# Kernel tuning notes

Hardware: AMD Instinct MI355X
Metric: run time of the kernel (lower is better)

The kernel has to match this reference:

```python
import jax, jax.numpy as jnp
import numpy as np
import math

C = 1.0          # Poincare ball curvature
MIN_NORM = 1e-15
BALL_EPS = 1e-5  # clamp for artanh args


def _norm(x):
    return jnp.sqrt(jnp.maximum(jnp.sum(x * x, -1, keepdims=True), MIN_NORM))


def expmap0(u, c=C):
    sc = jnp.sqrt(c)
    n = _norm(u)
    return jnp.tanh(sc * n) * u / (sc * n)


def logmap0(x, c=C):
    sc = jnp.sqrt(c)
    n = _norm(x)
    return jnp.arctanh(jnp.minimum(sc * n, 1.0 - BALL_EPS)) * x / (sc * n)


def mobius_add(x, y, c=C):
    x2 = jnp.sum(x * x, -1, keepdims=True)
    y2 = jnp.sum(y * y, -1, keepdims=True)
    xy = jnp.sum(x * y, -1, keepdims=True)
    num = (1.0 + 2.0 * c * xy + c * y2) * x + (1.0 - c * x2) * y
    den = 1.0 + 2.0 * c * xy + c * c * x2 * y2
    return num / jnp.maximum(den, MIN_NORM)


def mobius_matvec(W, x, c=C):
    # W: (out, in), x: (..., in)
    sc = jnp.sqrt(c)
    xn = _norm(x)
    mx = x @ W.T
    mxn = _norm(mx)
    return jnp.tanh(mxn / xn * jnp.arctanh(jnp.minimum(sc * xn, 1.0 - BALL_EPS))) * mx / (mxn * sc)


def mobius_scalar_mul(r, x, c=C):
    sc = jnp.sqrt(c)
    n = _norm(x)
    return jnp.tanh(r * jnp.arctanh(jnp.minimum(sc * n, 1.0 - BALL_EPS))) * x / (n * sc)


def hyp_linear(x, W, b):
    return mobius_add(mobius_matvec(W, x), b)


def layer_norm(t, w, b, eps=1e-5):
    mu = jnp.mean(t, -1, keepdims=True)
    var = jnp.mean((t - mu) ** 2, -1, keepdims=True)
    return (t - mu) / jnp.sqrt(var + eps) * w + b


def hyp_layer_norm(x, w, b):
    return expmap0(layer_norm(logmap0(x), w, b))


def _hyperbolic_attention_scores(q, k, c=C, epsilon=1e-15, delta=1e-7):
    # q, k: (B, H, S, Dh)
    max_norm = (1.0 - 1e-5) / math.sqrt(c)
    q = jnp.minimum(q, max_norm)  # elementwise clamp_max, faithful to torch
    k = jnp.minimum(k, max_norm)
    q_norm_sq = c * jnp.sum(q * q, -1, keepdims=True)          # (B,H,Sq,1)
    k_norm_sq = c * jnp.sum(k * k, -1, keepdims=True)          # (B,H,Sk,1)
    # diff: (B,H,Sq,Sk,Dh) = mobius_add(-k, q) pairwise
    diff = mobius_add(-k[:, :, None, :, :], q[:, :, :, None, :], c)
    diff_norm_sq = c * jnp.sum(diff * diff, -1)                # (B,H,Sq,Sk)
    denom = (1.0 - q_norm_sq) * (1.0 - jnp.swapaxes(k_norm_sq, 2, 3)) + epsilon
    acosh_arg = 1.0 + 2.0 * diff_norm_sq / denom
    acosh_arg = jnp.maximum(acosh_arg, 1.0 + delta)
    dist = jnp.log(acosh_arg + jnp.sqrt(acosh_arg * acosh_arg - 1.0))
    return -dist


def setup_inputs() -> dict:
    key = jax.random.key(0)
    D, H, FF = 768, 12, 4 * 768
    B, S = 2, 196
    ks = jax.random.split(key, 8)

    def xavier(k, out_f, in_f):
        lim = math.sqrt(6.0 / (in_f + out_f))
        return jax.random.uniform(k, (out_f, in_f), jnp.float32, -lim, lim)

    x = jax.random.normal(ks[0], (B, S, D), jnp.float32) * 0.02  # inside unit ball
    return {
        "x": x,
        "wq": xavier(ks[1], D, D), "bq": jnp.zeros((D,), jnp.float32),
        "wk": xavier(ks[2], D, D), "bk": jnp.zeros((D,), jnp.float32),
        "wv": xavier(ks[3], D, D), "bv": jnp.zeros((D,), jnp.float32),
        "wo": xavier(ks[4], D, D), "bo": jnp.zeros((D,), jnp.float32),
        "head_scaling": jnp.ones((H, 1, 1), jnp.float32),
        "w1": xavier(ks[5], FF, D), "b1": jnp.zeros((FF,), jnp.float32),
        "w2": xavier(ks[6], D, FF), "b2": jnp.zeros((D,), jnp.float32),
        "beta": jnp.ones((1,), jnp.float32),
        "ln1_w": jnp.ones((D,), jnp.float32), "ln1_b": jnp.zeros((D,), jnp.float32),
        "ln2_w": jnp.ones((D,), jnp.float32), "ln2_b": jnp.zeros((D,), jnp.float32),
    }


def reference(x, wq, bq, wk, bk, wv, bv, wo, bo, head_scaling,
              w1, b1, w2, b2, beta, ln1_w, ln1_b, ln2_w, ln2_b):
    B, S, D = x.shape
    H = head_scaling.shape[0]
    Dh = D // H

    # --- hyperbolic multi-head attention ---
    q = hyp_linear(x, wq, bq)
    k = hyp_linear(x, wk, bk)
    v = hyp_linear(x, wv, bv)
    q = jnp.transpose(q.reshape(B, S, H, Dh), (0, 2, 1, 3))
    k = jnp.transpose(k.reshape(B, S, H, Dh), (0, 2, 1, 3))
    v = jnp.transpose(v.reshape(B, S, H, Dh), (0, 2, 1, 3))

    scores = _hyperbolic_attention_scores(q, k) / (head_scaling * math.sqrt(Dh))
    attn = jax.nn.softmax(scores, axis=-1)                       # (B,H,Sq,Sk)
    attn_out = expmap0(jnp.einsum('bhqk,bhkd->bhqd', attn, logmap0(v)))
    attn_out = jnp.transpose(attn_out, (0, 2, 1, 3)).reshape(B, S, D)
    attn_out = hyp_linear(attn_out, wo, bo)

    # --- residual 1 + hyperbolic layer norm ---
    h = mobius_add(x, mobius_scalar_mul(beta, attn_out))
    h = hyp_layer_norm(h, ln1_w, ln1_b)

    # --- mobius FFN ---
    f = hyp_linear(h, w1, b1)
    f = expmap0(jax.nn.relu(logmap0(f)))   # mobius_relu
    f = hyp_linear(f, w2, b2)

    # --- residual 2 + hyperbolic layer norm ---
    out = mobius_add(h, mobius_scalar_mul(beta, f))
    out = hyp_layer_norm(out, ln2_w, ln2_b)
    return out
```

## Files before the change

kernel.cpp:

```cpp
#include <hip/hip_runtime.h>
#include <hip/hip_bf16.h>
#include <math.h>

#define BATCH 2
#define SEQ 196
#define DMODEL 768
#define NHEAD 12
#define DHEAD 64
#define DFF 3072
#define NROWS (BATCH*SEQ)
#define NBH   (BATCH*NHEAD)
#define NHROWS (NBH*SEQ)

typedef __attribute__((ext_vector_type(8))) short short8;
typedef __attribute__((ext_vector_type(4))) float f32x4;

__device__ __forceinline__ short f2bf(float f) {
  unsigned u = __builtin_bit_cast(unsigned, f);
  u += 0x7FFFu + ((u >> 16) & 1u);
  return (short)(u >> 16);
}
__device__ __forceinline__ float bf2f(short s) {
  unsigned u = ((unsigned)(unsigned short)s) << 16;
  return __builtin_bit_cast(float, u);
}
__device__ __forceinline__ float wave_sum64(float v) {
  #pragma unroll
  for (int off = 32; off; off >>= 1) v += __shfl_xor(v, off);
  return v;
}

__device__ __forceinline__ void block_reduce_sum4(float& a, float& b, float& c, float& d,
                                                  float* sbuf ) {
  #pragma unroll
  for (int off = 32; off; off >>= 1) {
    a += __shfl_xor(a, off);
    b += __shfl_xor(b, off);
    c += __shfl_xor(c, off);
    d += __shfl_xor(d, off);
  }
  int wid = threadIdx.x >> 6;
  if ((threadIdx.x & 63) == 0) {
    sbuf[wid*4+0] = a; sbuf[wid*4+1] = b; sbuf[wid*4+2] = c; sbuf[wid*4+3] = d;
  }
  __syncthreads();
  a = sbuf[0] + sbuf[4] + sbuf[8]  + sbuf[12];
  b = sbuf[1] + sbuf[5] + sbuf[9]  + sbuf[13];
  c = sbuf[2] + sbuf[6] + sbuf[10] + sbuf[14];
  d = sbuf[3] + sbuf[7] + sbuf[11] + sbuf[15];
  __syncthreads();
}

#define PITCH 72

__global__ __launch_bounds__(256) void gemm_qkv_f32(
    const float* __restrict__ X,
    const float* __restrict__ Wq, const float* __restrict__ Wk, const float* __restrict__ Wv,
    float* __restrict__ Yq, float* __restrict__ Yk, float* __restrict__ Yv) {
  const float* W = Wq; float* Y = Yq;
  if (blockIdx.z == 1) { W = Wk; Y = Yk; }
  else if (blockIdx.z == 2) { W = Wv; Y = Yv; }
  const int K = DMODEL, m = DMODEL, n = NROWS;

  __shared__ short As[64*PITCH];
  __shared__ short Bs[64*PITCH];
  const int tid  = threadIdx.x;
  const int lane = tid & 63;
  const int w    = tid >> 6, wr = w >> 1, wc = w & 1;
  const int brow = blockIdx.y * 64, bcol = blockIdx.x * 64;

  const int sr = tid >> 2, sc = (tid & 3) * 16;
  const bool rok = (brow + sr) < n;
  const float* xp = X + (size_t)(brow + sr) * K + sc;
  const float* wp = W + (size_t)(bcol + sr) * K + sc;

  f32x4 acc[2][2] = {};
  const int kgo = (lane >> 4) * 8;
  const f32x4 zf = {0.f,0.f,0.f,0.f};

  f32x4 xa[4], wa[4];
  #pragma unroll
  for (int q = 0; q < 4; ++q) {
    xa[q] = rok ? *(const f32x4*)(xp + q*4) : zf;
    wa[q] = *(const f32x4*)(wp + q*4);
  }

  const int T = K / 64;
  for (int t = 0; t < T; ++t) {
    f32x4 xn[4], wn[4];
    const int kn = (t + 1 < T) ? (t + 1) * 64 : 0;
    #pragma unroll
    for (int q = 0; q < 4; ++q) {
      xn[q] = rok ? *(const f32x4*)(xp + kn + q*4) : zf;
      wn[q] = *(const f32x4*)(wp + kn + q*4);
    }

    short8 xs0, xs1, ws0, ws1;
    #pragma unroll
    for (int j = 0; j < 4; ++j) {
      xs0[j] = f2bf(xa[0][j]); xs0[j+4] = f2bf(xa[1][j]);
      xs1[j] = f2bf(xa[2][j]); xs1[j+4] = f2bf(xa[3][j]);
      ws0[j] = f2bf(wa[0][j]); ws0[j+4] = f2bf(wa[1][j]);
      ws1[j] = f2bf(wa[2][j]); ws1[j+4] = f2bf(wa[3][j]);
    }
    __syncthreads();
    *(short8*)&As[sr*PITCH + sc]     = xs0;
    *(short8*)&As[sr*PITCH + sc + 8] = xs1;
    *(short8*)&Bs[sr*PITCH + sc]     = ws0;
    *(short8*)&Bs[sr*PITCH + sc + 8] = ws1;
    __syncthreads();

    #pragma unroll
    for (int kk = 0; kk < 2; ++kk) {
      short8 a0 = *(const short8*)&As[(wr*32      + (lane & 15))*PITCH + kk*32 + kgo];
      short8 a1 = *(const short8*)&As[(wr*32 + 16 + (lane & 15))*PITCH + kk*32 + kgo];
      short8 b0 = *(const short8*)&Bs[(wc*32      + (lane & 15))*PITCH + kk*32 + kgo];
      short8 b1 = *(const short8*)&Bs[(wc*32 + 16 + (lane & 15))*PITCH + kk*32 + kgo];
      acc[0][0] = __builtin_amdgcn_mfma_f32_16x16x32_bf16(a0, b0, acc[0][0], 0, 0, 0);
      acc[0][1] = __builtin_amdgcn_mfma_f32_16x16x32_bf16(a0, b1, acc[0][1], 0, 0, 0);
      acc[1][0] = __builtin_amdgcn_mfma_f32_16x16x32_bf16(a1, b0, acc[1][0], 0, 0, 0);
      acc[1][1] = __builtin_amdgcn_mfma_f32_16x16x32_bf16(a1, b1, acc[1][1], 0, 0, 0);
    }
    #pragma unroll
    for (int q = 0; q < 4; ++q) { xa[q] = xn[q]; wa[q] = wn[q]; }
  }

  const int ccol = bcol + wc*32 + (lane & 15);
  #pragma unroll
  for (int mr = 0; mr < 2; ++mr) {
    #pragma unroll
    for (int j = 0; j < 4; ++j) {
      int grow = brow + wr*32 + mr*16 + (lane >> 4)*4 + j;
      if (grow < n) {
        float* yr = Y + (size_t)grow * m + ccol;
        yr[0]  = acc[mr][0][j];
        yr[16] = acc[mr][1][j];
      }
    }
  }
}

__global__ __launch_bounds__(256) void gemm_awf32(
    const short* __restrict__ A, const float* __restrict__ W,
    float* __restrict__ Yparts, int n, int Ktot, int m, int KK) {
  const int z = blockIdx.z;
  const int kbase = z * KK;
  float* Y = Yparts + (size_t)z * n * m;

  __shared__ short As[64*PITCH];
  __shared__ short Bs[64*PITCH];
  const int tid  = threadIdx.x;
  const int lane = tid & 63;
  const int w    = tid >> 6, wr = w >> 1, wc = w & 1;
  const int brow = blockIdx.y * 64, bcol = blockIdx.x * 64;

  const int sr = tid >> 2, sc = (tid & 3) * 16;
  const bool rok = (brow + sr) < n;
  const short* ap = A + (size_t)(brow + sr) * Ktot + kbase + sc;
  const float* wp = W + (size_t)(bcol + sr) * Ktot + kbase + sc;

  f32x4 acc[2][2] = {};
  const int kgo = (lane >> 4) * 8;
  const short8 z8 = {0,0,0,0,0,0,0,0};
  const f32x4 zf = {0.f,0.f,0.f,0.f};

  short8 aa0, aa1;
  f32x4 wa[4];
  if (rok) { aa0 = *(const short8*)(ap); aa1 = *(const short8*)(ap + 8); }
  else     { aa0 = z8; aa1 = z8; }
  #pragma unroll
  for (int q = 0; q < 4; ++q) wa[q] = *(const f32x4*)(wp + q*4);

  const int T = KK / 64;
  for (int t = 0; t < T; ++t) {
    short8 an0, an1;
    f32x4 wn[4];
    const int kn = (t + 1 < T) ? (t + 1) * 64 : 0;
    if (rok) { an0 = *(const short8*)(ap + kn); an1 = *(const short8*)(ap + kn + 8); }
    else     { an0 = z8; an1 = z8; }
    #pragma unroll
    for (int q = 0; q < 4; ++q) wn[q] = *(const f32x4*)(wp + kn + q*4);

    short8 ws0, ws1;
    #pragma unroll
    for (int j = 0; j < 4; ++j) {
      ws0[j] = f2bf(wa[0][j]); ws0[j+4] = f2bf(wa[1][j]);
      ws1[j] = f2bf(wa[2][j]); ws1[j+4] = f2bf(wa[3][j]);
    }
    __syncthreads();
    *(short8*)&As[sr*PITCH + sc]     = aa0;
    *(short8*)&As[sr*PITCH + sc + 8] = aa1;
    *(short8*)&Bs[sr*PITCH + sc]     = ws0;
    *(short8*)&Bs[sr*PITCH + sc + 8] = ws1;
    __syncthreads();

    #pragma unroll
    for (int kk = 0; kk < 2; ++kk) {
      short8 a0 = *(const short8*)&As[(wr*32      + (lane & 15))*PITCH + kk*32 + kgo];
      short8 a1 = *(const short8*)&As[(wr*32 + 16 + (lane & 15))*PITCH + kk*32 + kgo];
      short8 b0 = *(const short8*)&Bs[(wc*32      + (lane & 15))*PITCH + kk*32 + kgo];
      short8 b1 = *(const short8*)&Bs[(wc*32 + 16 + (lane & 15))*PITCH + kk*32 + kgo];
      acc[0][0] = __builtin_amdgcn_mfma_f32_16x16x32_bf16(a0, b0, acc[0][0], 0, 0, 0);
      acc[0][1] = __builtin_amdgcn_mfma_f32_16x16x32_bf16(a0, b1, acc[0][1], 0, 0, 0);
      acc[1][0] = __builtin_amdgcn_mfma_f32_16x16x32_bf16(a1, b0, acc[1][0], 0, 0, 0);
      acc[1][1] = __builtin_amdgcn_mfma_f32_16x16x32_bf16(a1, b1, acc[1][1], 0, 0, 0);
    }
    aa0 = an0; aa1 = an1;
    #pragma unroll
    for (int q = 0; q < 4; ++q) wa[q] = wn[q];
  }

  const int ccol = bcol + wc*32 + (lane & 15);
  #pragma unroll
  for (int mr = 0; mr < 2; ++mr) {
    #pragma unroll
    for (int j = 0; j < 4; ++j) {
      int grow = brow + wr*32 + mr*16 + (lane >> 4)*4 + j;
      if (grow < n) {
        float* yr = Y + (size_t)grow * m + ccol;
        yr[0]  = acc[mr][0][j];
        yr[16] = acc[mr][1][j];
      }
    }
  }
}

#define P_P 256
__global__ __launch_bounds__(256) void qkv_post(const float* __restrict__ X,
                                                const float* __restrict__ MQ,
                                                const float* __restrict__ MK,
                                                const float* __restrict__ MV,
                                                const float* __restrict__ bq,
                                                const float* __restrict__ bk,
                                                const float* __restrict__ bv,
                                                short* __restrict__ qhb,
                                                short* __restrict__ khb,
                                                float* __restrict__ q2s,
                                                float* __restrict__ k2s,
                                                short* __restrict__ lvT) {
  __shared__ float sbuf[16];
  const int r = blockIdx.x;
  const int b = r / SEQ, s = r % SEQ;
  const int y = blockIdx.y;
  const float* MX   = (y == 0) ? MQ : (y == 1) ? MK : MV;
  const float* bias = (y == 0) ? bq : (y == 1) ? bk : bv;
  const float* xr = X + (size_t)r*DMODEL;
  const float* mr = MX + (size_t)r*DMODEL;
  const int tid = threadIdx.x, wid = tid >> 6, lane = tid & 63;
  const float maxn = 1.0f - 1e-5f;

  float xs = 0.f, ms = 0.f, mb = 0.f, bb = 0.f;
  float mv[3], bvv[3];
  #pragma unroll
  for (int l = 0; l < 3; ++l) {
    int i = tid + l*256;
    float xv = xr[i];
    mv[l] = mr[i]; bvv[l] = bias[i];
    xs += xv*xv; ms += mv[l]*mv[l]; mb += mv[l]*bvv[l]; bb += bvv[l]*bvv[l];
  }
  block_reduce_sum4(xs, ms, mb, bb, sbuf);
  float xn  = sqrtf(fmaxf(xs, 1e-15f));
  float mxn = sqrtf(fmaxf(ms, 1e-15f));
  float art = atanhf(fminf(xn, maxn));
  float scm = tanhf(mxn/xn*art)/mxn;
  float x2 = scm*scm*ms;
  float y2 = bb;
  float xy = scm*mb;
  float den = fmaxf(1.f + 2.f*xy + x2*y2, 1e-15f);
  float ca = (1.f + 2.f*xy + y2) * scm / den;
  float cb = (1.f - x2) / den;

  #pragma unroll
  for (int l = 0; l < 3; ++l) {
    float o = ca*mv[l] + cb*bvv[l];
    int h = l*4 + wid;
    size_t hr = (size_t)(b*NHEAD + h)*SEQ + s;
    if (y < 2) {
      short c16 = f2bf(fminf(o, maxn));
      float cf = bf2f(c16);
      float nn = wave_sum64(cf*cf);
      if (y == 0) {
        qhb[hr*64 + lane] = c16;
        if (lane == 0) q2s[hr] = nn;
      } else {
        khb[hr*64 + lane] = c16;
        if (lane == 0) k2s[hr] = nn;
      }
    } else {
      float nn = wave_sum64(o*o);
      float n = sqrtf(fmaxf(nn, 1e-15f));
      float scl = atanhf(fminf(n, maxn))/n;
      lvT[((size_t)(b*NHEAD + h)*DHEAD + lane)*P_P + s] = f2bf(scl*o);
    }
  }
}

#define SP 72
#define PP 264
__global__ __launch_bounds__(256) void attn_mfma(
    const short* __restrict__ qhb, const short* __restrict__ khb,
    const float* __restrict__ q2s, const float* __restrict__ k2s,
    const short* __restrict__ lvT, const float* __restrict__ hs,
    short* __restrict__ aob) {
  __shared__ __align__(16) char smem[9216 + 224*SP*2];
  __shared__ float q2l[64];
  __shared__ float k2l[224];
  __shared__ float redA[64][2];
  __shared__ float redB[64][2];

  const int tile = blockIdx.x, bh = blockIdx.z;
  const int h = bh % NHEAD, b = bh / NHEAD;
  const int i0 = tile*64;
  const int tid = threadIdx.x, lane = tid & 63, w = tid >> 6, wr = w >> 1, wc = w & 1;
  short* Qs = (short*)smem;
  short* Ks = (short*)(smem + 9216);
  short* Pl = (short*)smem;
  const short8 z8 = {0,0,0,0,0,0,0,0};
  const int kgo = (lane >> 4)*8;

  {
    int row = tid >> 2, seg = (tid & 3)*16;
    int gr = i0 + row;
    short8 v0 = z8, v1 = z8;
    if (gr < SEQ) {
      const short* p = qhb + ((size_t)bh*SEQ + gr)*64 + seg;
      v0 = *(const short8*)p; v1 = *(const short8*)(p + 8);
    }
    *(short8*)&Qs[row*SP + seg]     = v0;
    *(short8*)&Qs[row*SP + seg + 8] = v1;
  }
  for (int u = tid; u < 224*4; u += 256) {
    int row = u >> 2, seg = (u & 3)*16;
    short8 v0 = z8, v1 = z8;
    if (row < SEQ) {
      const short* p = khb + ((size_t)bh*SEQ + row)*64 + seg;
      v0 = *(const short8*)p; v1 = *(const short8*)(p + 8);
    }
    *(short8*)&Ks[row*SP + seg]     = v0;
    *(short8*)&Ks[row*SP + seg + 8] = v1;
  }
  if (tid < 64)  q2l[tid] = (i0 + tid < SEQ) ? q2s[(size_t)bh*SEQ + i0 + tid] : 0.f;
  if (tid < 224) k2l[tid] = (tid < SEQ) ? k2s[(size_t)bh*SEQ + tid] : 0.f;
  __syncthreads();

  f32x4 acc[2][7] = {};
  #pragma unroll
  for (int kk = 0; kk < 2; ++kk) {
    short8 a0 = *(const short8*)&Qs[(wr*32      + (lane & 15))*SP + kk*32 + kgo];
    short8 a1 = *(const short8*)&Qs[(wr*32 + 16 + (lane & 15))*SP + kk*32 + kgo];
// ... 5 lines not shown
    }
  }

  const float inv_hsv = 1.f/(hs[h]*8.0f);
  #pragma unroll
  for (int rf = 0; rf < 2; ++rf) {
    #pragma unroll
    for (int j = 0; j < 4; ++j) {
      int rl = wr*32 + rf*16 + (lane >> 4)*4 + j;
      float q2 = q2l[rl];
      #pragma unroll
      for (int cf = 0; cf < 7; ++cf) {
        int col = wc*112 + cf*16 + (lane & 15);
        float kq = acc[rf][cf][j];
        float k2 = k2l[col];
        float xy = -kq;
        float al = 1.f + 2.f*xy + q2;
        float be = 1.f - k2;
        float num2 = al*al*k2 + 2.f*al*be*xy + be*be*q2;
        float den  = fmaxf(1.f + 2.f*xy + k2*q2, 1e-15f);
        float dns  = num2/(den*den);
        float denom = (1.f - q2)*(1.f - k2) + 1e-15f;
        float arg = fmaxf(1.f + 2.f*dns/denom, 1.f + 1e-7f);
        float dist = logf(arg + sqrtf(arg*arg - 1.f));
        acc[rf][cf][j] = (col < SEQ) ? -dist*inv_hsv : -1e30f;
      }
      float m = acc[rf][0][j];
      #pragma unroll
      for (int cf = 1; cf < 7; ++cf) m = fmaxf(m, acc[rf][cf][j]);
      m = fmaxf(m, __shfl_xor(m, 1));
      m = fmaxf(m, __shfl_xor(m, 2));
      m = fmaxf(m, __shfl_xor(m, 4));
      m = fmaxf(m, __shfl_xor(m, 8));
      if ((lane & 15) == 0) redA[rl][wc] = m;
    }
  }
  __syncthreads();

  #pragma unroll
  for (int rf = 0; rf < 2; ++rf) {
    #pragma unroll
    for (int j = 0; j < 4; ++j) {
      int rl = wr*32 + rf*16 + (lane >> 4)*4 + j;
      float m = fmaxf(redA[rl][0], redA[rl][1]);
      float s = 0.f;
      #pragma unroll
      for (int cf = 0; cf < 7; ++cf) {
        float e = expf(acc[rf][cf][j] - m);
        acc[rf][cf][j] = e;
        s += e;
      }
      s += __shfl_xor(s, 1); s += __shfl_xor(s, 2);
      s += __shfl_xor(s, 4); s += __shfl_xor(s, 8);
      if ((lane & 15) == 0) redB[rl][wc] = s;
    }
  }
  __syncthreads();

  #pragma unroll
  for (int rf = 0; rf < 2; ++rf) {
    #pragma unroll
    for (int j = 0; j < 4; ++j) {
      int rl = wr*32 + rf*16 + (lane >> 4)*4 + j;
      float inv = 1.f/(redB[rl][0] + redB[rl][1]);
      #pragma unroll
      for (int cf = 0; cf < 7; ++cf) {
        int col = wc*112 + cf*16 + (lane & 15);
        Pl[rl*PP + col] = f2bf(acc[rf][cf][j]*inv);
      }
    }
  }
  __syncthreads();

  f32x4 acc2[2][2] = {};
  const short* lvb = lvT + (size_t)bh*DHEAD*P_P;
  #pragma unroll
  for (int ks = 0; ks < 7; ++ks) {
    short8 a0 = *(const short8*)&Pl[(wr*32      + (lane & 15))*PP + ks*32 + kgo];
    short8 a1 = *(const short8*)&Pl[(wr*32 + 16 + (lane & 15))*PP + ks*32 + kgo];
    short8 b0 = *(const short8*)(lvb + (size_t)(wc*32      + (lane & 15))*P_P + ks*32 + kgo);
    short8 b1 = *(const short8*)(lvb + (size_t)(wc*32 + 16 + (lane & 15))*P_P + ks*32 + kgo);
    acc2[0][0] = __builtin_amdgcn_mfma_f32_16x16x32_bf16(a0, b0, acc2[0][0], 0, 0, 0);
    acc2[0][1] = __builtin_amdgcn_mfma_f32_16x16x32_bf16(a0, b1, acc2[0][1], 0, 0, 0);
    acc2[1][0] = __builtin_amdgcn_mfma_f32_16x16x32_bf16(a1, b0, acc2[1][0], 0, 0, 0);
    acc2[1][1] = __builtin_amdgcn_mfma_f32_16x16x32_bf16(a1, b1, acc2[1][1], 0, 0, 0);
  }

  #pragma unroll
  for (int rf = 0; rf < 2; ++rf) {
    #pragma unroll
    for (int j = 0; j < 4; ++j) {
      int rl = wr*32 + rf*16 + (lane >> 4)*4 + j;
      float s = acc2[rf][0][j]*acc2[rf][0][j] + acc2[rf][1][j]*acc2[rf][1][j];
      s += __shfl_xor(s, 1); s += __shfl_xor(s, 2);
      s += __shfl_xor(s, 4); s += __shfl_xor(s, 8);
      if ((lane & 15) == 0) redA[rl][wc] = s;
    }
  }
  __syncthreads();

  #pragma unroll
  for (int rf = 0; rf < 2; ++rf) {
    #pragma unroll
    for (int j = 0; j < 4; ++j) {
      int rl = wr*32 + rf*16 + (lane >> 4)*4 + j;
      int grow = i0 + rl;
      if (grow < SEQ) {
        float n2 = redA[rl][0] + redA[rl][1];
        float n = sqrtf(fmaxf(n2, 1e-15f));
        float scl = tanhf(n)/n;
        #pragma unroll
        for (int cf2 = 0; cf2 < 2; ++cf2) {
          int col = h*64 + wc*32 + cf2*16 + (lane & 15);
          float o = scl*acc2[rf][cf2][j];
          aob[(size_t)(b*SEQ + grow)*DMODEL + col] = f2bf(o);
        }
      }
    }
  }
}

__global__ __launch_bounds__(256) void post_resid_ln(
    const short* __restrict__ Xbf, const float* __restrict__ xsArr, int din,
    const float* __restrict__ MXp, int nparts,
    const float* __restrict__ bias, const float* __restrict__ RX,
    const float* __restrict__ betap, const float* __restrict__ lnw,
    const float* __restrict__ lnb,
    float* __restrict__ out, short* __restrict__ outb) {
  __shared__ float sbuf[16];
  const int r = blockIdx.x;
  const int tid = threadIdx.x;

  float xs = 0.f, ms = 0.f, mb = 0.f, bb = 0.f;
  float mv[3], bvv[3];
  #pragma unroll
  for (int l = 0; l < 3; ++l) {
    int i = tid + l*256;
    float acc = 0.f;
    for (int p = 0; p < nparts; ++p)
      acc += MXp[(size_t)p*NROWS*DMODEL + (size_t)r*DMODEL + i];
    mv[l] = acc; bvv[l] = bias[i];
    ms += mv[l]*mv[l]; mb += mv[l]*bvv[l]; bb += bvv[l]*bvv[l];
  }
  if (Xbf) {
    const short* xr = Xbf + (size_t)r*din;
    for (int i = tid; i < din; i += 256) { float v = bf2f(xr[i]); xs += v*v; }
  }
  block_reduce_sum4(xs, ms, mb, bb, sbuf);
  if (!Xbf) xs = xsArr[r];

  float xn  = sqrtf(fmaxf(xs, 1e-15f));
  float mxn = sqrtf(fmaxf(ms, 1e-15f));
  float art = atanhf(fminf(xn, 1.f - 1e-5f));
  float scm = tanhf(mxn/xn*art)/mxn;
  float px2 = scm*scm*ms;
  float py2 = bb;
  float pxy = scm*mb;
  float pden = fmaxf(1.f + 2.f*pxy + px2*py2, 1e-15f);
  float pca = (1.f + 2.f*pxy + py2) * scm / pden;
  float pcb = (1.f - px2) / pden;

  const float* xr2 = RX + (size_t)r*DMODEL;
  float xv[3], yv[3];
// ... 22 lines not shown
  float z1 = 0.f, z2 = 0.f, z3 = 0.f;
  block_reduce_sum4(h2, z1, z2, z3, sbuf);

  float nh = sqrtf(fmaxf(h2, 1e-15f));
  float scl = atanhf(fminf(nh, 1.f - 1e-5f))/nh;
  float tv[3]; float tsum = 0.f, tsq = 0.f;
  #pragma unroll
  for (int l = 0; l < 3; ++l) { tv[l] = scl*hv[l]; tsum += tv[l]; tsq += tv[l]*tv[l]; }
  float zz = 0.f, zw = 0.f;
  block_reduce_sum4(tsum, tsq, zz, zw, sbuf);
  float mu  = tsum * (1.f/768.f);
  float var = tsq * (1.f/768.f) - mu*mu;
  float rstd = rsqrtf(var + 1e-5f);
  float lnv[3]; float l2 = 0.f;
  #pragma unroll
  for (int l = 0; l < 3; ++l) {
    int i = tid + l*256;
    lnv[l] = (tv[l] - mu)*rstd*lnw[i] + lnb[i];
    l2 += lnv[l]*lnv[l];
  }
  float w1 = 0.f, w2 = 0.f, w3 = 0.f;
  block_reduce_sum4(l2, w1, w2, w3, sbuf);
  float nl = sqrtf(fmaxf(l2, 1e-15f));
  float sce = tanhf(nl)/nl;
  #pragma unroll
  for (int l = 0; l < 3; ++l) {
    int i = tid + l*256;
    float o = sce*lnv[l];
    out[(size_t)r*DMODEL + i] = o;
    if (outb) outb[(size_t)r*DMODEL + i] = f2bf(o);
  }
}

__global__ __launch_bounds__(256) void ffn1_post(const float* __restrict__ hb,
                                                 const float* __restrict__ MX,
                                                 const float* __restrict__ bias,
                                                 short* __restrict__ fbb,
                                                 float* __restrict__ fnorm) {
  __shared__ float sbuf[16];
  const int r = blockIdx.x;
  const int tid = threadIdx.x;
  const float* xr = hb + (size_t)r*DMODEL;
  const float* mr = MX + (size_t)r*DFF;

  float xs = 0.f, ms = 0.f, mb = 0.f, bb = 0.f;
  float mv[12], bvv[12];
  for (int i = tid; i < DMODEL; i += 256) { float v = xr[i]; xs += v*v; }
  #pragma unroll
  for (int l = 0; l < 12; ++l) {
    int i = tid + l*256;
    mv[l] = mr[i]; bvv[l] = bias[i];
    ms += mv[l]*mv[l]; mb += mv[l]*bvv[l]; bb += bvv[l]*bvv[l];
  }
  block_reduce_sum4(xs, ms, mb, bb, sbuf);
  float xn  = sqrtf(fmaxf(xs, 1e-15f));
  float mxn = sqrtf(fmaxf(ms, 1e-15f));
  float art = atanhf(fminf(xn, 1.f - 1e-5f));
  float scm = tanhf(mxn/xn*art)/mxn;
  float px2 = scm*scm*ms;
  float py2 = bb;
  float pxy = scm*mb;
  float pden = fmaxf(1.f + 2.f*pxy + px2*py2, 1e-15f);
  float pca = (1.f + 2.f*pxy + py2) * scm / pden;
  float pcb = (1.f - px2) / pden;

  float s2 = pca*pca*ms + 2.f*pca*pcb*mb + pcb*pcb*bb;
  float n = sqrtf(fmaxf(s2, 1e-15f));
  float scl = atanhf(fminf(n, 1.f - 1e-5f))/n;
  float rv[12]; float r2 = 0.f;
  #pragma unroll
  for (int l = 0; l < 12; ++l) {
    float f = pca*mv[l] + pcb*bvv[l];
    rv[l] = fmaxf(scl*f, 0.f);
    r2 += rv[l]*rv[l];
  }
  float w1 = 0.f, w2 = 0.f, w3 = 0.f;
  block_reduce_sum4(r2, w1, w2, w3, sbuf);
  float nr = sqrtf(fmaxf(r2, 1e-15f));
  float sce = tanhf(nr)/nr;
  #pragma unroll
  for (int l = 0; l < 12; ++l)
    fbb[(size_t)r*DFF + tid + l*256] = f2bf(sce*rv[l]);
  if (tid == 0) fnorm[r] = sce*sce*r2;
}

extern "C" void kernel_launch(void* const* d_in, const int* in_sizes, int n_in,
                              void* d_out, int out_size, void* d_ws, size_t ws_size,
                              hipStream_t stream) {
  const float* x    = (const float*)d_in[0];
  const float* wq   = (const float*)d_in[1];
  const float* bq   = (const float*)d_in[2];
  const float* wk   = (const float*)d_in[3];
  const float* bk   = (const float*)d_in[4];
  const float* wv   = (const float*)d_in[5];
  const float* bv   = (const float*)d_in[6];
  const float* wo   = (const float*)d_in[7];
  const float* bo   = (const float*)d_in[8];
  const float* hs   = (const float*)d_in[9];
  const float* w1   = (const float*)d_in[10];
  const float* b1   = (const float*)d_in[11];
  const float* w2   = (const float*)d_in[12];
  const float* b2   = (const float*)d_in[13];
  const float* beta = (const float*)d_in[14];
  const float* ln1w = (const float*)d_in[15];
  const float* ln1b = (const float*)d_in[16];
  const float* ln2w = (const float*)d_in[17];
  const float* ln2b = (const float*)d_in[18];
  float* out = (float*)d_out;

  char* base = (char*)d_ws;
  size_t off = 0;
  auto allocB = [&](size_t bytes) {
    off = (off + 63) & ~(size_t)63;
    void* p = base + off; off += bytes; return p;
  };
  short* aob  = (short*)allocB((size_t)NROWS*DMODEL * 2);
  short* hbb  = (short*)allocB((size_t)NROWS*DMODEL * 2);
  short* fbb  = (short*)allocB((size_t)NROWS*DFF * 2);
  float* tq   = (float*)allocB((size_t)NROWS*DMODEL * 4);
  float* tk   = (float*)allocB((size_t)NROWS*DMODEL * 4);
  float* tv   = (float*)allocB((size_t)NROWS*DMODEL * 4);
  float* gparts = (float*)allocB((size_t)4*NROWS*DMODEL * 4);
  short* qhb  = (short*)allocB((size_t)NHROWS*DHEAD * 2);
  short* khb  = (short*)allocB((size_t)NHROWS*DHEAD * 2);
  float* q2s  = (float*)allocB((size_t)NHROWS * 4);
  float* k2s  = (float*)allocB((size_t)NHROWS * 4);
  short* lvT  = (short*)allocB((size_t)NBH*DHEAD*P_P * 2);
  float* hb   = (float*)allocB((size_t)NROWS*DMODEL * 4);
  float* tmpF = (float*)allocB((size_t)NROWS*DFF * 4);
  float* fnorm= (float*)allocB((size_t)NROWS * 4);

  dim3 blk(256);
  dim3 gQKV(DMODEL/64, (NROWS+63)/64, 3);
  dim3 gO(DMODEL/64,   (NROWS+63)/64, 2);
  dim3 gF1(DFF/64,     (NROWS+63)/64, 1);
  dim3 gF2(DMODEL/64,  (NROWS+63)/64, 4);
  dim3 gATT(4, 1, NBH);

  gemm_qkv_f32<<<gQKV, blk, 0, stream>>>(x, wq, wk, wv, tq, tk, tv);
  qkv_post<<<dim3(NROWS, 3), blk, 0, stream>>>(x, tq, tk, tv, bq, bk, bv,
                                               qhb, khb, q2s, k2s, lvT);

  attn_mfma<<<gATT, blk, 0, stream>>>(qhb, khb, q2s, k2s, lvT, hs, aob);

  gemm_awf32<<<gO, blk, 0, stream>>>(aob, wo, gparts, NROWS, DMODEL, DMODEL, DMODEL/2);
  post_resid_ln<<<NROWS, blk, 0, stream>>>(aob, nullptr, DMODEL, gparts, 2, bo, x,
                                           beta, ln1w, ln1b, hb, hbb);

  gemm_awf32<<<gF1, blk, 0, stream>>>(hbb, w1, tmpF, NROWS, DMODEL, DFF, DMODEL);
  ffn1_post<<<NROWS, blk, 0, stream>>>(hb, tmpF, b1, fbb, fnorm);
  gemm_awf32<<<gF2, blk, 0, stream>>>(fbb, w2, gparts, NROWS, DFF, DMODEL, DFF/4);
  post_resid_ln<<<NROWS, blk, 0, stream>>>(nullptr, fnorm, DFF, gparts, 4, b2, hb,
                                           beta, ln2w, ln2b, out, nullptr);
}
```

Baseline: 111.6 us.

## Merge all stages into one cooperative persistent kernel with grid syncs

```diff
diff --git a/kernel.cpp b/kernel.cpp
--- a/kernel.cpp
+++ b/kernel.cpp
@@ -1,6 +1,9 @@
 #include <hip/hip_runtime.h>
 #include <hip/hip_bf16.h>
+#include <hip/hip_cooperative_groups.h>
 #include <math.h>
+
+namespace cg = cooperative_groups;
 
 #define BATCH 2
 #define SEQ 196
@@ -52,22 +55,19 @@
 }
 
 #define PITCH 72
-
-__global__ __launch_bounds__(256) void gemm_qkv_f32(
-    const float* __restrict__ X,
-    const float* __restrict__ Wq, const float* __restrict__ Wk, const float* __restrict__ Wv,
-    float* __restrict__ Yq, float* __restrict__ Yk, float* __restrict__ Yv) {
-  const float* W = Wq; float* Y = Yq;
-  if (blockIdx.z == 1) { W = Wk; Y = Yk; }
-  else if (blockIdx.z == 2) { W = Wv; Y = Yv; }
+#define P_P 256
+#define SP 72
+#define PP 264
+
+__device__ void gemm_qkv_tile(const float* __restrict__ X, const float* __restrict__ W,
+                              float* __restrict__ Y, int bx, int by, char* U) {
+  short* As = (short*)U;
+  short* Bs = (short*)(U + 9216);
   const int K = DMODEL, m = DMODEL, n = NROWS;
-
-  __shared__ short As[64*PITCH];
-  __shared__ short Bs[64*PITCH];
   const int tid  = threadIdx.x;
   const int lane = tid & 63;
   const int w    = tid >> 6, wr = w >> 1, wc = w & 1;
-  const int brow = blockIdx.y * 64, bcol = blockIdx.x * 64;
+  const int brow = by * 64, bcol = bx * 64;
 
   const int sr = tid >> 2, sc = (tid & 3) * 16;
   const bool rok = (brow + sr) < n;
@@ -140,19 +140,15 @@
   }
 }
 
-__global__ __launch_bounds__(256) void gemm_awf32(
-    const short* __restrict__ A, const float* __restrict__ W,
-    float* __restrict__ Yparts, int n, int Ktot, int m, int KK) {
-  const int z = blockIdx.z;
-  const int kbase = z * KK;
-  float* Y = Yparts + (size_t)z * n * m;
-
-  __shared__ short As[64*PITCH];
-  __shared__ short Bs[64*PITCH];
+__device__ void gemm_awf32_tile(const short* __restrict__ A, const float* __restrict__ W,
+                                float* __restrict__ Y, int n, int Ktot, int m,
+                                int kbase, int KK, int bx, int by, char* U) {
+  short* As = (short*)U;
+  short* Bs = (short*)(U + 9216);
   const int tid  = threadIdx.x;
   const int lane = tid & 63;
   const int w    = tid >> 6, wr = w >> 1, wc = w & 1;
-  const int brow = blockIdx.y * 64, bcol = blockIdx.x * 64;
+  const int brow = by * 64, bcol = bx * 64;
 
   const int sr = tid >> 2, sc = (tid & 3) * 16;
   const bool rok = (brow + sr) < n;
@@ -162,7 +158,6 @@
   f32x4 acc[2][2] = {};
   const int kgo = (lane >> 4) * 8;
   const short8 z8 = {0,0,0,0,0,0,0,0};
-  const f32x4 zf = {0.f,0.f,0.f,0.f};
 
   short8 aa0, aa1;
   f32x4 wa[4];
@@ -225,25 +220,12 @@
   }
 }
 
-#define P_P 256
-__global__ __launch_bounds__(256) void qkv_post(const float* __restrict__ X,
-                                                const float* __restrict__ MQ,
-                                                const float* __restrict__ MK,
-                                                const float* __restrict__ MV,
-                                                const float* __restrict__ bq,
-                                                const float* __restrict__ bk,
-                                                const float* __restrict__ bv,
-                                                short* __restrict__ qhb,
-                                                short* __restrict__ khb,
-                                                float* __restrict__ q2s,
-                                                float* __restrict__ k2s,
-                                                short* __restrict__ lvT) {
-  __shared__ float sbuf[16];
-  const int r = blockIdx.x;
+__device__ void qkv_post_row(const float* __restrict__ X, const float* __restrict__ MX,
+                             const float* __restrict__ bias,
+                             short* __restrict__ qhb, short* __restrict__ khb,
+                             float* __restrict__ q2s, float* __restrict__ k2s,
+                             short* __restrict__ lvT, int r, int y, float* sbuf) {
   const int b = r / SEQ, s = r % SEQ;
-  const int y = blockIdx.y;
-  const float* MX   = (y == 0) ? MQ : (y == 1) ? MK : MV;
-  const float* bias = (y == 0) ? bq : (y == 1) ? bk : bv;
   const float* xr = X + (size_t)r*DMODEL;
   const float* mr = MX + (size_t)r*DMODEL;
   const int tid = threadIdx.x, wid = tid >> 6, lane = tid & 63;
@@ -295,26 +277,21 @@
   }
 }
 
-#define SP 72
-#define PP 264
-__global__ __launch_bounds__(256) void attn_mfma(
-    const short* __restrict__ qhb, const short* __restrict__ khb,
-    const float* __restrict__ q2s, const float* __restrict__ k2s,
-    const short* __restrict__ lvT, const float* __restrict__ hs,
-    short* __restrict__ aob) {
-  __shared__ __align__(16) char smem[9216 + 224*SP*2];
-  __shared__ float q2l[64];
-  __shared__ float k2l[224];
-  __shared__ float redA[64][2];
-  __shared__ float redB[64][2];
-
-  const int tile = blockIdx.x, bh = blockIdx.z;
+__device__ void attn_tile(const short* __restrict__ qhb, const short* __restrict__ khb,
+                          const float* __restrict__ q2s, const float* __restrict__ k2s,
+                          const short* __restrict__ lvT, const float* __restrict__ hs,
+                          short* __restrict__ aob, int tile, int bh, char* U) {
+  short* Qs = (short*)U;
+  short* Ks = (short*)(U + 9216);
+  short* Pl = (short*)U;
+  float* q2l  = (float*)(U + 41472);
+  float* k2l  = (float*)(U + 41728);
+  float* redA = (float*)(U + 42624);
+  float* redB = (float*)(U + 43136);
+
   const int h = bh % NHEAD, b = bh / NHEAD;
   const int i0 = tile*64;
   const int tid = threadIdx.x, lane = tid & 63, w = tid >> 6, wr = w >> 1, wc = w & 1;
-  short* Qs = (short*)smem;
-  short* Ks = (short*)(smem + 9216);
-  short* Pl = (short*)smem;
   const short8 z8 = {0,0,0,0,0,0,0,0};
   const int kgo = (lane >> 4)*8;
 
@@ -386,7 +363,7 @@
       m = fmaxf(m, __shfl_xor(m, 2));
       m = fmaxf(m, __shfl_xor(m, 4));
       m = fmaxf(m, __shfl_xor(m, 8));
-      if ((lane & 15) == 0) redA[rl][wc] = m;
+      if ((lane & 15) == 0) redA[rl*2 + wc] = m;
     }
   }
   __syncthreads();
@@ -396,7 +373,7 @@
     #pragma unroll
     for (int j = 0; j < 4; ++j) {
       int rl = wr*32 + rf*16 + (lane >> 4)*4 + j;
-      float m = fmaxf(redA[rl][0], redA[rl][1]);
+      float m = fmaxf(redA[rl*2], redA[rl*2 + 1]);
       float s = 0.f;
       #pragma unroll
       for (int cf = 0; cf < 7; ++cf) {
@@ -406,7 +383,7 @@
       }
       s += __shfl_xor(s, 1); s += __shfl_xor(s, 2);
       s += __shfl_xor(s, 4); s += __shfl_xor(s, 8);
-      if ((lane & 15) == 0) redB[rl][wc] = s;
+      if ((lane & 15) == 0) redB[rl*2 + wc] = s;
     }
   }
   __syncthreads();
@@ -416,7 +393,7 @@
     #pragma unroll
     for (int j = 0; j < 4; ++j) {
       int rl = wr*32 + rf*16 + (lane >> 4)*4 + j;
-      float inv = 1.f/(redB[rl][0] + redB[rl][1]);
+      float inv = 1.f/(redB[rl*2] + redB[rl*2 + 1]);
       #pragma unroll
       for (int cf = 0; cf < 7; ++cf) {
         int col = wc*112 + cf*16 + (lane & 15);
@@ -448,7 +425,7 @@
       float s = acc2[rf][0][j]*acc2[rf][0][j] + acc2[rf][1][j]*acc2[rf][1][j];
       s += __shfl_xor(s, 1); s += __shfl_xor(s, 2);
       s += __shfl_xor(s, 4); s += __shfl_xor(s, 8);
-      if ((lane & 15) == 0) redA[rl][wc] = s;
+      if ((lane & 15) == 0) redA[rl*2 + wc] = s;
     }
   }
   __syncthreads();
@@ -460,7 +437,7 @@
       int rl = wr*32 + rf*16 + (lane >> 4)*4 + j;
       int grow = i0 + rl;
       if (grow < SEQ) {
-        float n2 = redA[rl][0] + redA[rl][1];
+        float n2 = redA[rl*2] + redA[rl*2 + 1];
         float n = sqrtf(fmaxf(n2, 1e-15f));
         float scl = tanhf(n)/n;
         #pragma unroll
@@ -472,17 +449,16 @@
       }
     }
   }
-}
-
-__global__ __launch_bounds__(256) void post_resid_ln(
+  __syncthreads();
+}
+
+__device__ void post_resid_ln_row(
     const short* __restrict__ Xbf, const float* __restrict__ xsArr, int din,
     const float* __restrict__ MXp, int nparts,
     const float* __restrict__ bias, const float* __restrict__ RX,
     const float* __restrict__ betap, const float* __restrict__ lnw,
     const float* __restrict__ lnb,
-    float* __restrict__ out, short* __restrict__ outb) {
-  __shared__ float sbuf[16];
-  const int r = blockIdx.x;
+    float* __restrict__ out, short* __restrict__ outb, int r, float* sbuf) {
   const int tid = threadIdx.x;
 
   float xs = 0.f, ms = 0.f, mb = 0.f, bb = 0.f;
@@ -571,13 +547,10 @@
   }
 }
 
-__global__ __launch_bounds__(256) void ffn1_post(const float* __restrict__ hb,
-                                                 const float* __restrict__ MX,
-                                                 const float* __restrict__ bias,
-                                                 short* __restrict__ fbb,
-                                                 float* __restrict__ fnorm) {
-  __shared__ float sbuf[16];
-  const int r = blockIdx.x;
+__device__ void ffn1_post_row(const float* __restrict__ hb, const float* __restrict__ MX,
+                              const float* __restrict__ bias,
+                              short* __restrict__ fbb, float* __restrict__ fnorm,
+                              int r, float* sbuf) {
   const int tid = threadIdx.x;
   const float* xr = hb + (size_t)r*DMODEL;
   const float* mr = MX + (size_t)r*DFF;
@@ -623,30 +596,80 @@
   if (tid == 0) fnorm[r] = sce*sce*r2;
 }
 
+struct MegaArgs {
+  const float *x, *wq, *bq, *wk, *bk, *wv, *bv, *wo, *bo, *hs;
+  const float *w1, *b1, *w2, *b2, *beta, *ln1w, *ln1b, *ln2w, *ln2b;
+  float* out;
+  short *aob, *hbb, *fbb;
+  float *tq, *tk, *tv, *gparts;
+  short *qhb, *khb;
+  float *q2s, *k2s;
+  short *lvT;
+  float *hb, *tmpF, *fnorm;
+};
+
+__global__ __launch_bounds__(256, 1) void mega_kernel(MegaArgs a) {
+  cg::grid_group grid = cg::this_grid();
+  __shared__ __align__(16) char U[43648];
+  float* sbuf = (float*)U;
+  const int bid = blockIdx.x;
+
+  if (bid < 252) {
+    int z = bid / 84, rem = bid % 84, bx = rem % 12, by = rem / 12;
+    const float* W = (z == 0) ? a.wq : (z == 1) ? a.wk : a.wv;
+    float* Y = (z == 0) ? a.tq : (z == 1) ? a.tk : a.tv;
+    gemm_qkv_tile(a.x, W, Y, bx, by, U);
+  }
+  grid.sync();
+
+  for (int j = bid; j < 1176; j += 256) {
+    int r = j % NROWS, y = j / NROWS;
+    const float* MX   = (y == 0) ? a.tq : (y == 1) ? a.tk : a.tv;
+    const float* bias = (y == 0) ? a.bq : (y == 1) ? a.bk : a.bv;
+    qkv_post_row(a.x, MX, bias, a.qhb, a.khb, a.q2s, a.k2s, a.lvT, r, y, sbuf);
+  }
+  grid.sync();
+
+  if (bid < 96) attn_tile(a.qhb, a.khb, a.q2s, a.k2s, a.lvT, a.hs, a.aob, bid % 4, bid / 4, U);
+  grid.sync();
+
+  if (bid < 168) {
+    int z = bid / 84, rem = bid % 84, bx = rem % 12, by = rem / 12;
+    gemm_awf32_tile(a.aob, a.wo, a.gparts + (size_t)z*NROWS*DMODEL,
+                    NROWS, DMODEL, DMODEL, z*(DMODEL/2), DMODEL/2, bx, by, U);
+  }
+  grid.sync();
+
+  for (int j = bid; j < NROWS; j += 256)
+    post_resid_ln_row(a.aob, nullptr, DMODEL, a.gparts, 2, a.bo, a.x,
+                      a.beta, a.ln1w, a.ln1b, a.hb, a.hbb, j, sbuf);
+  grid.sync();
+
+  for (int j = bid; j < 336; j += 256) {
+    int bx = j % 48, by = j / 48;
+    gemm_awf32_tile(a.hbb, a.w1, a.tmpF, NROWS, DMODEL, DFF, 0, DMODEL, bx, by, U);
+  }
+  grid.sync();
+
+  for (int j = bid; j < NROWS; j += 256)
+    ffn1_post_row(a.hb, a.tmpF, a.b1, a.fbb, a.fnorm, j, sbuf);
+  grid.sync();
+
+  for (int j = bid; j < 336; j += 256) {
+    int z = j / 84, rem = j % 84, bx = rem % 12, by = rem / 12;
+    gemm_awf32_tile(a.fbb, a.w2, a.gparts + (size_t)z*NROWS*DMODEL,
+                    NROWS, DFF, DMODEL, z*(DFF/4), DFF/4, bx, by, U);
+  }
+  grid.sync();
+
+  for (int j = bid; j < NROWS; j += 256)
+    post_resid_ln_row(nullptr, a.fnorm, DFF, a.gparts, 4, a.b2, a.hb,
+                      a.beta, a.ln2w, a.ln2b, a.out, nullptr, j, sbuf);
+}
+
 extern "C" void kernel_launch(void* const* d_in, const int* in_sizes, int n_in,
                               void* d_out, int out_size, void* d_ws, size_t ws_size,
                               hipStream_t stream) {
-  const float* x    = (const float*)d_in[0];
-  const float* wq   = (const float*)d_in[1];
-  const float* bq   = (const float*)d_in[2];
-  const float* wk   = (const float*)d_in[3];
-  const float* bk   = (const float*)d_in[4];
-  const float* wv   = (const float*)d_in[5];
-  const float* bv   = (const float*)d_in[6];
-  const float* wo   = (const float*)d_in[7];
-  const float* bo   = (const float*)d_in[8];
-  const float* hs   = (const float*)d_in[9];
-  const float* w1   = (const float*)d_in[10];
-  const float* b1   = (const float*)d_in[11];
-  const float* w2   = (const float*)d_in[12];
-  const float* b2   = (const float*)d_in[13];
-  const float* beta = (const float*)d_in[14];
-  const float* ln1w = (const float*)d_in[15];
-  const float* ln1b = (const float*)d_in[16];
-  const float* ln2w = (const float*)d_in[17];
-  const float* ln2b = (const float*)d_in[18];
-  float* out = (float*)d_out;
-
   char* base = (char*)d_ws;
   size_t off = 0;
   auto allocB = [&](size_t bytes) {
@@ -669,26 +692,32 @@
   float* tmpF = (float*)allocB((size_t)NROWS*DFF * 4);
   float* fnorm= (float*)allocB((size_t)NROWS * 4);
 
-  dim3 blk(256);
-  dim3 gQKV(DMODEL/64, (NROWS+63)/64, 3);
-  dim3 gO(DMODEL/64,   (NROWS+63)/64, 2);
-  dim3 gF1(DFF/64,     (NROWS+63)/64, 1);
-  dim3 gF2(DMODEL/64,  (NROWS+63)/64, 4);
-  dim3 gATT(4, 1, NBH);
-
-  gemm_qkv_f32<<<gQKV, blk, 0, stream>>>(x, wq, wk, wv, tq, tk, tv);
-  qkv_post<<<dim3(NROWS, 3), blk, 0, stream>>>(x, tq, tk, tv, bq, bk, bv,
-                                               qhb, khb, q2s, k2s, lvT);
-
-  attn_mfma<<<gATT, blk, 0, stream>>>(qhb, khb, q2s, k2s, lvT, hs, aob);
-
-  gemm_awf32<<<gO, blk, 0, stream>>>(aob, wo, gparts, NROWS, DMODEL, DMODEL, DMODEL/2);
-  post_resid_ln<<<NROWS, blk, 0, stream>>>(aob, nullptr, DMODEL, gparts, 2, bo, x,
-                                           beta, ln1w, ln1b, hb, hbb);
-
-  gemm_awf32<<<gF1, blk, 0, stream>>>(hbb, w1, tmpF, NROWS, DMODEL, DFF, DMODEL);
-  ffn1_post<<<NROWS, blk, 0, stream>>>(hb, tmpF, b1, fbb, fnorm);
-  gemm_awf32<<<gF2, blk, 0, stream>>>(fbb, w2, gparts, NROWS, DFF, DMODEL, DFF/4);
-  post_resid_ln<<<NROWS, blk, 0, stream>>>(nullptr, fnorm, DFF, gparts, 4, b2, hb,
-                                           beta, ln2w, ln2b, out, nullptr);
-}
+  MegaArgs a;
+  a.x    = (const float*)d_in[0];
+  a.wq   = (const float*)d_in[1];
+  a.bq   = (const float*)d_in[2];
+  a.wk   = (const float*)d_in[3];
+  a.bk   = (const float*)d_in[4];
+  a.wv   = (const float*)d_in[5];
+  a.bv   = (const float*)d_in[6];
+  a.wo   = (const float*)d_in[7];
+  a.bo   = (const float*)d_in[8];
+  a.hs   = (const float*)d_in[9];
+  a.w1   = (const float*)d_in[10];
+  a.b1   = (const float*)d_in[11];
+  a.w2   = (const float*)d_in[12];
+  a.b2   = (const float*)d_in[13];
+  a.beta = (const float*)d_in[14];
+  a.ln1w = (const float*)d_in[15];
+  a.ln1b = (const float*)d_in[16];
+  a.ln2w = (const float*)d_in[17];
+  a.ln2b = (const float*)d_in[18];
+  a.out  = (float*)d_out;
+  a.aob = aob; a.hbb = hbb; a.fbb = fbb;
+  a.tq = tq; a.tk = tk; a.tv = tv; a.gparts = gparts;
+  a.qhb = qhb; a.khb = khb; a.q2s = q2s; a.k2s = k2s; a.lvT = lvT;
+  a.hb = hb; a.tmpF = tmpF; a.fnorm = fnorm;
+
+  void* params[] = { &a };
+  hipLaunchCooperativeKernel((void*)mega_kernel, dim3(256), dim3(256), params, 0, stream);
+}
```

Result: slower. 395.0 us (+253.8%).

## Split-K the QKV and FFN1 GEMMs and widen the K tile in gemm_awf32

Applied to the files above, without the earlier changes.

```diff
diff --git a/kernel.cpp b/kernel.cpp
--- a/kernel.cpp
+++ b/kernel.cpp
@@ -52,15 +52,17 @@
 }
 
 #define PITCH 72
+#define PITCH2 136
 
 __global__ __launch_bounds__(256) void gemm_qkv_f32(
     const float* __restrict__ X,
     const float* __restrict__ Wq, const float* __restrict__ Wk, const float* __restrict__ Wv,
-    float* __restrict__ Yq, float* __restrict__ Yk, float* __restrict__ Yv) {
-  const float* W = Wq; float* Y = Yq;
-  if (blockIdx.z == 1) { W = Wk; Y = Yk; }
-  else if (blockIdx.z == 2) { W = Wv; Y = Yv; }
+    float* __restrict__ parts) {
+  const int z = blockIdx.z, mat = z >> 1, slice = z & 1;
+  const float* W = (mat == 0) ? Wq : (mat == 1) ? Wk : Wv;
+  float* Y = parts + (size_t)z * NROWS * DMODEL;
   const int K = DMODEL, m = DMODEL, n = NROWS;
+  const int kbase = slice * (DMODEL/2);
 
   __shared__ short As[64*PITCH];
   __shared__ short Bs[64*PITCH];
@@ -71,8 +73,8 @@
 
   const int sr = tid >> 2, sc = (tid & 3) * 16;
   const bool rok = (brow + sr) < n;
-  const float* xp = X + (size_t)(brow + sr) * K + sc;
-  const float* wp = W + (size_t)(bcol + sr) * K + sc;
+  const float* xp = X + (size_t)(brow + sr) * K + kbase + sc;
+  const float* wp = W + (size_t)(bcol + sr) * K + kbase + sc;
 
   f32x4 acc[2][2] = {};
   const int kgo = (lane >> 4) * 8;
@@ -85,7 +87,7 @@
     wa[q] = *(const f32x4*)(wp + q*4);
   }
 
-  const int T = K / 64;
+  const int T = (DMODEL/2) / 64;
   for (int t = 0; t < T; ++t) {
     f32x4 xn[4], wn[4];
     const int kn = (t + 1 < T) ? (t + 1) * 64 : 0;
@@ -147,14 +149,14 @@
   const int kbase = z * KK;
   float* Y = Yparts + (size_t)z * n * m;
 
-  __shared__ short As[64*PITCH];
-  __shared__ short Bs[64*PITCH];
+  __shared__ short As[64*PITCH2];
+  __shared__ short Bs[64*PITCH2];
   const int tid  = threadIdx.x;
   const int lane = tid & 63;
   const int w    = tid >> 6, wr = w >> 1, wc = w & 1;
   const int brow = blockIdx.y * 64, bcol = blockIdx.x * 64;
 
-  const int sr = tid >> 2, sc = (tid & 3) * 16;
+  const int sr = tid >> 2, sc = (tid & 3) * 32;
   const bool rok = (brow + sr) < n;
   const short* ap = A + (size_t)(brow + sr) * Ktot + kbase + sc;
   const float* wp = W + (size_t)(bcol + sr) * Ktot + kbase + sc;
@@ -162,52 +164,56 @@
   f32x4 acc[2][2] = {};
   const int kgo = (lane >> 4) * 8;
   const short8 z8 = {0,0,0,0,0,0,0,0};
-  const f32x4 zf = {0.f,0.f,0.f,0.f};
-
-  short8 aa0, aa1;
-  f32x4 wa[4];
-  if (rok) { aa0 = *(const short8*)(ap); aa1 = *(const short8*)(ap + 8); }
-  else     { aa0 = z8; aa1 = z8; }
-  #pragma unroll
-  for (int q = 0; q < 4; ++q) wa[q] = *(const f32x4*)(wp + q*4);
-
-  const int T = KK / 64;
+
+  short8 aa[4];
+  f32x4 wa[8];
+  #pragma unroll
+  for (int q = 0; q < 4; ++q) aa[q] = rok ? *(const short8*)(ap + q*8) : z8;
+  #pragma unroll
+  for (int q = 0; q < 8; ++q) wa[q] = *(const f32x4*)(wp + q*4);
+
+  const int T = KK / 128;
   for (int t = 0; t < T; ++t) {
-    short8 an0, an1;
-    f32x4 wn[4];
-    const int kn = (t + 1 < T) ? (t + 1) * 64 : 0;
-    if (rok) { an0 = *(const short8*)(ap + kn); an1 = *(const short8*)(ap + kn + 8); }
-    else     { an0 = z8; an1 = z8; }
-    #pragma unroll
-    for (int q = 0; q < 4; ++q) wn[q] = *(const f32x4*)(wp + kn + q*4);
-
-    short8 ws0, ws1;
-    #pragma unroll
-    for (int j = 0; j < 4; ++j) {
-      ws0[j] = f2bf(wa[0][j]); ws0[j+4] = f2bf(wa[1][j]);
-      ws1[j] = f2bf(wa[2][j]); ws1[j+4] = f2bf(wa[3][j]);
+    short8 an[4];
+    f32x4 wn[8];
+    const int kn = (t + 1 < T) ? (t + 1) * 128 : 0;
+    #pragma unroll
+    for (int q = 0; q < 4; ++q) an[q] = rok ? *(const short8*)(ap + kn + q*8) : z8;
+    #pragma unroll
+    for (int q = 0; q < 8; ++q) wn[q] = *(const f32x4*)(wp + kn + q*4);
+
+    short8 ws[4];
+    #pragma unroll
+    for (int s = 0; s < 4; ++s) {
+      #pragma unroll
+      for (int j = 0; j < 4; ++j) {
+        ws[s][j]   = f2bf(wa[2*s][j]);
+        ws[s][j+4] = f2bf(wa[2*s+1][j]);
+      }
     }
     __syncthreads();
-    *(short8*)&As[sr*PITCH + sc]     = aa0;
-    *(short8*)&As[sr*PITCH + sc + 8] = aa1;
-    *(short8*)&Bs[sr*PITCH + sc]     = ws0;
-    *(short8*)&Bs[sr*PITCH + sc + 8] = ws1;
+    #pragma unroll
+    for (int s = 0; s < 4; ++s) {
+      *(short8*)&As[sr*PITCH2 + sc + s*8] = aa[s];
+      *(short8*)&Bs[sr*PITCH2 + sc + s*8] = ws[s];
+    }
     __syncthreads();
 
     #pragma unroll
-    for (int kk = 0; kk < 2; ++kk) {
-      short8 a0 = *(const short8*)&As[(wr*32      + (lane & 15))*PITCH + kk*32 + kgo];
-      short8 a1 = *(const short8*)&As[(wr*32 + 16 + (lane & 15))*PITCH + kk*32 + kgo];
-      short8 b0 = *(const short8*)&Bs[(wc*32      + (lane & 15))*PITCH + kk*32 + kgo];
-      short8 b1 = *(const short8*)&Bs[(wc*32 + 16 + (lane & 15))*PITCH + kk*32 + kgo];
+    for (int kk = 0; kk < 4; ++kk) {
+      short8 a0 = *(const short8*)&As[(wr*32      + (lane & 15))*PITCH2 + kk*32 + kgo];
+      short8 a1 = *(const short8*)&As[(wr*32 + 16 + (lane & 15))*PITCH2 + kk*32 + kgo];
+      short8 b0 = *(const short8*)&Bs[(wc*32      + (lane & 15))*PITCH2 + kk*32 + kgo];
+      short8 b1 = *(const short8*)&Bs[(wc*32 + 16 + (lane & 15))*PITCH2 + kk*32 + kgo];
       acc[0][0] = __builtin_amdgcn_mfma_f32_16x16x32_bf16(a0, b0, acc[0][0], 0, 0, 0);
       acc[0][1] = __builtin_amdgcn_mfma_f32_16x16x32_bf16(a0, b1, acc[0][1], 0, 0, 0);
       acc[1][0] = __builtin_amdgcn_mfma_f32_16x16x32_bf16(a1, b0, acc[1][0], 0, 0, 0);
       acc[1][1] = __builtin_amdgcn_mfma_f32_16x16x32_bf16(a1, b1, acc[1][1], 0, 0, 0);
     }
-    aa0 = an0; aa1 = an1;
-    #pragma unroll
-    for (int q = 0; q < 4; ++q) wa[q] = wn[q];
+    #pragma unroll
+    for (int q = 0; q < 4; ++q) aa[q] = an[q];
+    #pragma unroll
+    for (int q = 0; q < 8; ++q) wa[q] = wn[q];
   }
 
   const int ccol = bcol + wc*32 + (lane & 15);
@@ -227,9 +233,7 @@
 
 #define P_P 256
 __global__ __launch_bounds__(256) void qkv_post(const float* __restrict__ X,
-                                                const float* __restrict__ MQ,
-                                                const float* __restrict__ MK,
-                                                const float* __restrict__ MV,
+                                                const float* __restrict__ parts,
                                                 const float* __restrict__ bq,
                                                 const float* __restrict__ bk,
                                                 const float* __restrict__ bv,
@@ -242,10 +246,10 @@
   const int r = blockIdx.x;
   const int b = r / SEQ, s = r % SEQ;
   const int y = blockIdx.y;
-  const float* MX   = (y == 0) ? MQ : (y == 1) ? MK : MV;
+  const float* p0 = parts + (size_t)(2*y)   * NROWS * DMODEL + (size_t)r*DMODEL;
+  const float* p1 = parts + (size_t)(2*y+1) * NROWS * DMODEL + (size_t)r*DMODEL;
   const float* bias = (y == 0) ? bq : (y == 1) ? bk : bv;
   const float* xr = X + (size_t)r*DMODEL;
-  const float* mr = MX + (size_t)r*DMODEL;
   const int tid = threadIdx.x, wid = tid >> 6, lane = tid & 63;
   const float maxn = 1.0f - 1e-5f;
 
@@ -255,7 +259,7 @@
   for (int l = 0; l < 3; ++l) {
     int i = tid + l*256;
     float xv = xr[i];
-    mv[l] = mr[i]; bvv[l] = bias[i];
+    mv[l] = p0[i] + p1[i]; bvv[l] = bias[i];
     xs += xv*xv; ms += mv[l]*mv[l]; mb += mv[l]*bvv[l]; bb += bvv[l]*bvv[l];
   }
   block_reduce_sum4(xs, ms, mb, bb, sbuf);
@@ -572,7 +576,7 @@
 }
 
 __global__ __launch_bounds__(256) void ffn1_post(const float* __restrict__ hb,
-                                                 const float* __restrict__ MX,
+                                                 const float* __restrict__ MXp,
                                                  const float* __restrict__ bias,
                                                  short* __restrict__ fbb,
                                                  float* __restrict__ fnorm) {
@@ -580,7 +584,8 @@
   const int r = blockIdx.x;
   const int tid = threadIdx.x;
   const float* xr = hb + (size_t)r*DMODEL;
-  const float* mr = MX + (size_t)r*DFF;
+  const float* mr0 = MXp + (size_t)r*DFF;
+  const float* mr1 = MXp + (size_t)NROWS*DFF + (size_t)r*DFF;
 
   float xs = 0.f, ms = 0.f, mb = 0.f, bb = 0.f;
   float mv[12], bvv[12];
@@ -588,7 +593,7 @@
   #pragma unroll
   for (int l = 0; l < 12; ++l) {
     int i = tid + l*256;
-    mv[l] = mr[i]; bvv[l] = bias[i];
+    mv[l] = mr0[i] + mr1[i]; bvv[l] = bias[i];
     ms += mv[l]*mv[l]; mb += mv[l]*bvv[l]; bb += bvv[l]*bvv[l];
   }
   block_reduce_sum4(xs, ms, mb, bb, sbuf);
@@ -656,28 +661,26 @@
   short* aob  = (short*)allocB((size_t)NROWS*DMODEL * 2);
   short* hbb  = (short*)allocB((size_t)NROWS*DMODEL * 2);
   short* fbb  = (short*)allocB((size_t)NROWS*DFF * 2);
-  float* tq   = (float*)allocB((size_t)NROWS*DMODEL * 4);
-  float* tk   = (float*)allocB((size_t)NROWS*DMODEL * 4);
-  float* tv   = (float*)allocB((size_t)NROWS*DMODEL * 4);
+  float* qparts = (float*)allocB((size_t)6*NROWS*DMODEL * 4);
   float* gparts = (float*)allocB((size_t)4*NROWS*DMODEL * 4);
+  float* tmpF2  = (float*)allocB((size_t)2*NROWS*DFF * 4);
   short* qhb  = (short*)allocB((size_t)NHROWS*DHEAD * 2);
   short* khb  = (short*)allocB((size_t)NHROWS*DHEAD * 2);
   float* q2s  = (float*)allocB((size_t)NHROWS * 4);
   float* k2s  = (float*)allocB((size_t)NHROWS * 4);
   short* lvT  = (short*)allocB((size_t)NBH*DHEAD*P_P * 2);
   float* hb   = (float*)allocB((size_t)NROWS*DMODEL * 4);
-  float* tmpF = (float*)allocB((size_t)NROWS*DFF * 4);
   float* fnorm= (float*)allocB((size_t)NROWS * 4);
 
   dim3 blk(256);
-  dim3 gQKV(DMODEL/64, (NROWS+63)/64, 3);
+  dim3 gQKV(DMODEL/64, (NROWS+63)/64, 6);
   dim3 gO(DMODEL/64,   (NROWS+63)/64, 2);
-  dim3 gF1(DFF/64,     (NROWS+63)/64, 1);
+  dim3 gF1(DFF/64,     (NROWS+63)/64, 2);
   dim3 gF2(DMODEL/64,  (NROWS+63)/64, 4);
   dim3 gATT(4, 1, NBH);
 
-  gemm_qkv_f32<<<gQKV, blk, 0, stream>>>(x, wq, wk, wv, tq, tk, tv);
-  qkv_post<<<dim3(NROWS, 3), blk, 0, stream>>>(x, tq, tk, tv, bq, bk, bv,
+  gemm_qkv_f32<<<gQKV, blk, 0, stream>>>(x, wq, wk, wv, qparts);
+  qkv_post<<<dim3(NROWS, 3), blk, 0, stream>>>(x, qparts, bq, bk, bv,
                                                qhb, khb, q2s, k2s, lvT);
 
   attn_mfma<<<gATT, blk, 0, stream>>>(qhb, khb, q2s, k2s, lvT, hs, aob);
@@ -686,8 +689,8 @@
   post_resid_ln<<<NROWS, blk, 0, stream>>>(aob, nullptr, DMODEL, gparts, 2, bo, x,
                                            beta, ln1w, ln1b, hb, hbb);
 
-  gemm_awf32<<<gF1, blk, 0, stream>>>(hbb, w1, tmpF, NROWS, DMODEL, DFF, DMODEL);
-  ffn1_post<<<NROWS, blk, 0, stream>>>(hb, tmpF, b1, fbb, fnorm);
+  gemm_awf32<<<gF1, blk, 0, stream>>>(hbb, w1, tmpF2, NROWS, DMODEL, DFF, DMODEL/2);
+  ffn1_post<<<NROWS, blk, 0, stream>>>(hb, tmpF2, b1, fbb, fnorm);
   gemm_awf32<<<gF2, blk, 0, stream>>>(fbb, w2, gparts, NROWS, DFF, DMODEL, DFF/4);
   post_resid_ln<<<NROWS, blk, 0, stream>>>(nullptr, fnorm, DFF, gparts, 4, b2, hb,
                                            beta, ln2w, ln2b, out, nullptr);
```

New measurement: 123.2 us. +10.3%, slower.
